# Kernel optimization log

Hardware: AMD Instinct MI355X
Metric: run time of the kernel (lower is better)

The kernel has to match this reference:

```python
import jax, jax.numpy as jnp
import numpy as np

N = 50000   # nodes
E = 600000  # edges (avg degree 12)
F = 16      # raw node features
P = 32      # n_channels_preproc
C = 128     # n_channels
L = 6       # n_gnn_layers
LBL = 2     # n_labels


def _dense_init(k, fan_in, shape):
    return (jax.random.normal(k, shape, jnp.float32) / np.float32(np.sqrt(fan_in)))


def setup_inputs() -> dict:
    key = jax.random.key(0)
    ks = jax.random.split(key, 12)
    return {
        "x": jax.random.normal(ks[0], (N, F), jnp.float32),
        "edge_src": jax.random.randint(ks[1], (E,), 0, N, dtype=jnp.int32),
        "edge_dst": jax.random.randint(ks[2], (E,), 0, N, dtype=jnp.int32),
        "edge_weight": jax.random.uniform(ks[3], (E,), jnp.float32),  # normalized-adjacency values
        "preproc_W": _dense_init(ks[4], F, (F, P)), "preproc_b": jnp.zeros((P,), jnp.float32),
        "fc_in1_W": _dense_init(ks[5], P, (P, C)), "fc_in1_b": jnp.zeros((C,), jnp.float32),
        "fc_in2_W": _dense_init(ks[6], P, (P, C)), "fc_in2_b": jnp.zeros((C,), jnp.float32),
        "gcn_W": _dense_init(ks[7], C, (L, C, C)), "gcn_b": jnp.zeros((L, C), jnp.float32),
        "fcg_W": _dense_init(ks[8], 2 * C, (L, 2 * C, C)), "fcg_b": jnp.zeros((L, C), jnp.float32),
        "last1_W": _dense_init(ks[9], 2 * C, (2 * C, C)), "last1_b": jnp.zeros((C,), jnp.float32),
        "last2_W": _dense_init(ks[10], C, (C, LBL)), "last2_b": jnp.zeros((LBL,), jnp.float32),
    }


def reference(x, edge_src, edge_dst, edge_weight,
              preproc_W, preproc_b, fc_in1_W, fc_in1_b, fc_in2_W, fc_in2_b,
              gcn_W, gcn_b, fcg_W, fcg_b, last1_W, last1_b, last2_W, last2_b):
    relu = jax.nn.relu
    h = relu(x @ preproc_W + preproc_b)                      # preproc Dense
    node_id = relu(h @ fc_in1_W + fc_in1_b)                  # node identity branch
    h = relu(h @ fc_in2_W + fc_in2_b)

    def layer(h, params):
        W, b, Wf, bf = params
        # GCNConv: act(A_hat @ (h @ W) + b), A_hat as COO edge list
        hw = h @ W                                           # [N, C]
        msg = hw[edge_src] * edge_weight[:, None]            # [E, C]
        agg = jax.ops.segment_sum(msg, edge_dst, num_segments=N)
        g = relu(agg + b)
        merged = jnp.concatenate([node_id, g], axis=-1)      # [N, 2C]
        return relu(merged @ Wf + bf), None                  # dropout = identity (eval)

    h, _ = jax.lax.scan(layer, h, (gcn_W, gcn_b, fcg_W, fcg_b))

    merged = jnp.concatenate([node_id, h], axis=-1)
    h = relu(merged @ last1_W + last1_b)
    return jax.nn.sigmoid(h @ last2_W + last2_b)             # [N, n_labels]
```

## Files before the change

kernel.cpp:

```cpp
#include <hip/hip_runtime.h>
#include <cstddef>
#include <cstdint>

#define NN 50000
#define NE 600000
#define SCAN_BLOCKS ((NN + 1023) / 1024)

typedef __attribute__((ext_vector_type(8))) short bf16x8;
typedef __attribute__((ext_vector_type(4))) float f32x4;

#define SWZ(x) (((x) ^ ((x) >> 2)) & 3)

__device__ __forceinline__ float bf2f(ushort u) {
    return __uint_as_float(((uint32_t)u) << 16);
}
__device__ __forceinline__ ushort f2bf(float f) {
    uint32_t b = __float_as_uint(f);
    return (ushort)((b + 0x7FFF + ((b >> 16) & 1)) >> 16);
}

__global__ __launch_bounds__(256)
void convert_weights(const float* __restrict__ f1W, const float* __restrict__ f2W,
                     const float* __restrict__ gW, const float* __restrict__ fgW,
                     const float* __restrict__ l1W, ushort* __restrict__ wt)
{
    int i = blockIdx.x * 256 + threadIdx.x;
    if (i >= 335872) return;
    float v;
    if (i < 4096) {
        int c = i >> 5, k = i & 31;
        v = f1W[k * 128 + c];
    } else if (i < 8192) {
        int j = i - 4096; int c = j >> 5, k = j & 31;
        v = f2W[k * 128 + c];
    } else if (i < 8192 + 98304) {
        int j = i - 8192; int l = j >> 14, r = j & 16383;
        int c = r >> 7, k = r & 127;
        v = gW[l * 16384 + k * 128 + c];
    } else if (i < 8192 + 98304 + 196608) {
        int j = i - (8192 + 98304); int l = j >> 15, r = j & 32767;
        int c = r >> 8, k = r & 255;
        v = fgW[l * 32768 + k * 128 + c];
    } else {
        int j = i - (8192 + 98304 + 196608);
        int c = j >> 8, k = j & 255;
        v = l1W[k * 128 + c];
    }
    wt[i] = f2bf(v);
}

__global__ __launch_bounds__(256)
void preproc_kernel(const float* __restrict__ x, const float* __restrict__ W,
                    const float* __restrict__ b, ushort* __restrict__ out)
{
    __shared__ float Wl[512];
    __shared__ float bl[32];
    int tx = threadIdx.x;
    Wl[tx]       = W[tx];
    Wl[tx + 256] = W[tx + 256];
    if (tx < 32) bl[tx] = b[tx];
    __syncthreads();
    int n = blockIdx.x * 256 + tx;
    if (n >= NN) return;
    float xr[16];
    const float4* xp = (const float4*)(x + (size_t)n * 16);
#pragma unroll
    for (int q = 0; q < 4; ++q) {
        float4 v = xp[q];
        xr[q*4+0]=v.x; xr[q*4+1]=v.y; xr[q*4+2]=v.z; xr[q*4+3]=v.w;
    }
    float acc[32];
#pragma unroll
    for (int c = 0; c < 32; ++c) acc[c] = bl[c];
#pragma unroll
    for (int k = 0; k < 16; ++k)
#pragma unroll
        for (int c = 0; c < 32; ++c)
            acc[c] = fmaf(xr[k], Wl[k*32+c], acc[c]);
    ushort4* op = (ushort4*)(out + (size_t)n * 32);
#pragma unroll
    for (int q = 0; q < 8; ++q) {
        ushort4 v;
        v.x = f2bf(fmaxf(acc[q*4+0], 0.f));
        v.y = f2bf(fmaxf(acc[q*4+1], 0.f));
        v.z = f2bf(fmaxf(acc[q*4+2], 0.f));
        v.w = f2bf(fmaxf(acc[q*4+3], 0.f));
        op[q] = v;
    }
}

__global__ __launch_bounds__(128)
void gemm_mfma(const ushort* __restrict__ A1, int K1,
               const ushort* __restrict__ Wt, const float* __restrict__ bias,
               ushort* __restrict__ out, int nrows)
{
    __shared__ ushort Atile[64 * 32];
    __shared__ ushort Btile[128 * 32];
    const int tx   = threadIdx.x;
    const int wave = tx >> 6;
    const int lane = tx & 63;
    const int bm   = blockIdx.x * 64;
    const int Ktot = K1;

    const int rs  = lane >> 2;
    const int chn = (lane & 3) ^ SWZ(rs);
    const int m    = lane & 15;
    const int quad = lane >> 4;
    const int slot = quad ^ SWZ(m);

    f32x4 acc0[8], acc1[8];
#pragma unroll
    for (int t = 0; t < 8; ++t) {
        acc0[t] = (f32x4){0.f, 0.f, 0.f, 0.f};
        acc1[t] = (f32x4){0.f, 0.f, 0.f, 0.f};
    }

    for (int kk = 0; kk < Ktot; kk += 32) {
#pragma unroll
        for (int i = 0; i < 2; ++i) {
            int seg = wave + 2 * i;
            int row = seg * 16 + rs;
            int ar  = bm + row; if (ar >= nrows) ar = nrows - 1;
            __builtin_amdgcn_global_load_lds(
                (const __attribute__((address_space(1))) void*)
                    (A1 + (size_t)ar * K1 + kk + chn * 8),
                (__attribute__((address_space(3))) void*)(Atile + seg * 512),
                16, 0, 0);
        }
#pragma unroll
        for (int i = 0; i < 4; ++i) {
            int seg = wave + 2 * i;
            int col = seg * 16 + rs;
            __builtin_amdgcn_global_load_lds(
                (const __attribute__((address_space(1))) void*)
                    (Wt + (size_t)col * Ktot + kk + chn * 8),
                (__attribute__((address_space(3))) void*)(Btile + seg * 512),
                16, 0, 0);
        }
        __syncthreads();
        bf16x8 af0 = *(const bf16x8*)(Atile + (wave * 32 + m) * 32 + slot * 8);
        bf16x8 af1 = *(const bf16x8*)(Atile + (wave * 32 + 16 + m) * 32 + slot * 8);
#pragma unroll
        for (int t = 0; t < 8; ++t) {
            bf16x8 bfr = *(const bf16x8*)(Btile + (t * 16 + m) * 32 + slot * 8);
            acc0[t] = __builtin_amdgcn_mfma_f32_16x16x32_bf16(af0, bfr, acc0[t], 0, 0, 0);
            acc1[t] = __builtin_amdgcn_mfma_f32_16x16x32_bf16(af1, bfr, acc1[t], 0, 0, 0);
        }
        __syncthreads();
    }

#pragma unroll
    for (int half = 0; half < 2; ++half) {
        const int orow0 = bm + wave * 32 + half * 16 + quad * 4;
#pragma unroll
        for (int t = 0; t < 8; ++t) {
            int col = t * 16 + m;
            float bb = bias[col];
            f32x4 a = half ? acc1[t] : acc0[t];
#pragma unroll
            for (int r = 0; r < 4; ++r) {
                int row = orow0 + r;
                if (row < nrows)
                    out[(size_t)row * 128 + col] = f2bf(fmaxf(a[r] + bb, 0.f));
            }
        }
    }
}

__global__ __launch_bounds__(128)
void gemm_fused(const ushort* __restrict__ A1, int K1,
                const ushort* __restrict__ A2, int K2,
                const ushort* __restrict__ Wt, const float* __restrict__ bias,
                const ushort* __restrict__ Wg,
                ushort* __restrict__ out_hw, int nrows)
{
    __shared__ ushort Atile[64 * 32];
    __shared__ ushort Btile[128 * 32];
    __shared__ ushort Xt[64 * 128];
    const int tx   = threadIdx.x;
    const int wave = tx >> 6;
    const int lane = tx & 63;
    const int bm   = blockIdx.x * 64;
    const int Ktot = K1 + K2;

    const int rs  = lane >> 2;
    const int chn = (lane & 3) ^ SWZ(rs);
    const int m    = lane & 15;
    const int quad = lane >> 4;
    const int slot = quad ^ SWZ(m);

    f32x4 acc0[8], acc1[8];
#pragma unroll
    for (int t = 0; t < 8; ++t) {
        acc0[t] = (f32x4){0.f, 0.f, 0.f, 0.f};
        acc1[t] = (f32x4){0.f, 0.f, 0.f, 0.f};
    }

    for (int kk = 0; kk < Ktot; kk += 32) {
        const ushort* asrc; int astr, kl;
        if (kk < K1) { asrc = A1; astr = K1; kl = kk; }
        else         { asrc = A2; astr = K2; kl = kk - K1; }
#pragma unroll
        for (int i = 0; i < 2; ++i) {
            int seg = wave + 2 * i;
            int row = seg * 16 + rs;
            int ar  = bm + row; if (ar >= nrows) ar = nrows - 1;
            __builtin_amdgcn_global_load_lds(
                (const __attribute__((address_space(1))) void*)
                    (asrc + (size_t)ar * astr + kl + chn * 8),
                (__attribute__((address_space(3))) void*)(Atile + seg * 512),
                16, 0, 0);
        }
#pragma unroll
        for (int i = 0; i < 4; ++i) {
            int seg = wave + 2 * i;
            int col = seg * 16 + rs;
            __builtin_amdgcn_global_load_lds(
                (const __attribute__((address_space(1))) void*)
                    (Wt + (size_t)col * Ktot + kk + chn * 8),
                (__attribute__((address_space(3))) void*)(Btile + seg * 512),
                16, 0, 0);
        }
        __syncthreads();
        bf16x8 af0 = *(const bf16x8*)(Atile + (wave * 32 + m) * 32 + slot * 8);
        bf16x8 af1 = *(const bf16x8*)(Atile + (wave * 32 + 16 + m) * 32 + slot * 8);
#pragma unroll
        for (int t = 0; t < 8; ++t) {
            bf16x8 bfr = *(const bf16x8*)(Btile + (t * 16 + m) * 32 + slot * 8);
            acc0[t] = __builtin_amdgcn_mfma_f32_16x16x32_bf16(af0, bfr, acc0[t], 0, 0, 0);
            acc1[t] = __builtin_amdgcn_mfma_f32_16x16x32_bf16(af1, bfr, acc1[t], 0, 0, 0);
        }
        __syncthreads();
    }

#pragma unroll
    for (int half = 0; half < 2; ++half) {
        int rbase = wave * 32 + half * 16 + quad * 4;
#pragma unroll
        for (int t = 0; t < 8; ++t) {
            int col = t * 16 + m;
            float bb = bias[col];
            int c32 = col >> 5, within = col & 7, ks = (col >> 3) & 3;
            f32x4 a = half ? acc1[t] : acc0[t];
#pragma unroll
            for (int r = 0; r < 4; ++r) {
                int row = rbase + r;
                int pos = ks ^ SWZ(row & 15);
                Xt[row * 128 + c32 * 32 + pos * 8 + within] =
                    f2bf(fmaxf(a[r] + bb, 0.f));
            }
        }
    }
#pragma unroll
    for (int t = 0; t < 8; ++t) {
        acc0[t] = (f32x4){0.f, 0.f, 0.f, 0.f};
        acc1[t] = (f32x4){0.f, 0.f, 0.f, 0.f};
    }
    __syncthreads();

    for (int c32 = 0; c32 < 4; ++c32) {
        int kk = c32 * 32;
#pragma unroll
        for (int i = 0; i < 4; ++i) {
            int seg = wave + 2 * i;
            int col = seg * 16 + rs;
            __builtin_amdgcn_global_load_lds(
                (const __attribute__((address_space(1))) void*)
                    (Wg + (size_t)col * 128 + kk + chn * 8),
                (__attribute__((address_space(3))) void*)(Btile + seg * 512),
                16, 0, 0);
        }
        __syncthreads();
        bf16x8 af0 = *(const bf16x8*)(Xt + (wave * 32 + m) * 128 + kk + slot * 8);
        bf16x8 af1 = *(const bf16x8*)(Xt + (wave * 32 + 16 + m) * 128 + kk + slot * 8);
#pragma unroll
        for (int t = 0; t < 8; ++t) {
            bf16x8 bfr = *(const bf16x8*)(Btile + (t * 16 + m) * 32 + slot * 8);
            acc0[t] = __builtin_amdgcn_mfma_f32_16x16x32_bf16(af0, bfr, acc0[t], 0, 0, 0);
            acc1[t] = __builtin_amdgcn_mfma_f32_16x16x32_bf16(af1, bfr, acc1[t], 0, 0, 0);
        }
        __syncthreads();
    }

#pragma unroll
    for (int half = 0; half < 2; ++half) {
        const int orow0 = bm + wave * 32 + half * 16 + quad * 4;
#pragma unroll
        for (int t = 0; t < 8; ++t) {
            int col = t * 16 + m;
            f32x4 a = half ? acc1[t] : acc0[t];
#pragma unroll
            for (int r = 0; r < 4; ++r) {
                int row = orow0 + r;
                if (row < nrows)
                    out_hw[(size_t)row * 128 + col] = f2bf(a[r]);
            }
        }
    }
}

__global__ __launch_bounds__(128)
void gemm_last(const ushort* __restrict__ nid, const ushort* __restrict__ agg,
               const ushort* __restrict__ Wt, const float* __restrict__ bias5,
               const ushort* __restrict__ Wl1, const float* __restrict__ l1b,
               const float* __restrict__ l2W, const float* __restrict__ l2b,
               float* __restrict__ out, int nrows)
{
    __shared__ ushort Atile[64 * 32];
    __shared__ ushort Btile[128 * 32];
    __shared__ ushort Xt[64 * 128];
    __shared__ float  w2s[256];
    const int tx   = threadIdx.x;
    const int wave = tx >> 6;
    const int lane = tx & 63;
    const int bm   = blockIdx.x * 64;

    w2s[tx]       = l2W[tx];
    w2s[tx + 128] = l2W[tx + 128];

    const int rs  = lane >> 2;
    const int chn = (lane & 3) ^ SWZ(rs);
    const int m    = lane & 15;
    const int quad = lane >> 4;
    const int slot = quad ^ SWZ(m);

    f32x4 acc0[8], acc1[8];
#pragma unroll
    for (int t = 0; t < 8; ++t) {
        acc0[t] = (f32x4){0.f, 0.f, 0.f, 0.f};
        acc1[t] = (f32x4){0.f, 0.f, 0.f, 0.f};
    }

    for (int kk = 0; kk < 256; kk += 32) {
        const ushort* asrc; int kl;
        if (kk < 128) { asrc = nid; kl = kk; }
        else          { asrc = agg; kl = kk - 128; }
#pragma unroll
        for (int i = 0; i < 2; ++i) {
            int seg = wave + 2 * i;
            int row = seg * 16 + rs;
            int ar  = bm + row; if (ar >= nrows) ar = nrows - 1;
            __builtin_amdgcn_global_load_lds(
                (const __attribute__((address_space(1))) void*)
                    (asrc + (size_t)ar * 128 + kl + chn * 8),
                (__attribute__((address_space(3))) void*)(Atile + seg * 512),
                16, 0, 0);
        }
#pragma unroll
        for (int i = 0; i < 4; ++i) {
            int seg = wave + 2 * i;
            int col = seg * 16 + rs;
            __builtin_amdgcn_global_load_lds(
                (const __attribute__((address_space(1))) void*)
                    (Wt + (size_t)col * 256 + kk + chn * 8),
                (__attribute__((address_space(3))) void*)(Btile + seg * 512),
                16, 0, 0);
        }
        __syncthreads();
        bf16x8 af0 = *(const bf16x8*)(Atile + (wave * 32 + m) * 32 + slot * 8);
        bf16x8 af1 = *(const bf16x8*)(Atile + (wave * 32 + 16 + m) * 32 + slot * 8);
#pragma unroll
        for (int t = 0; t < 8; ++t) {
            bf16x8 bfr = *(const bf16x8*)(Btile + (t * 16 + m) * 32 + slot * 8);
            acc0[t] = __builtin_amdgcn_mfma_f32_16x16x32_bf16(af0, bfr, acc0[t], 0, 0, 0);
            acc1[t] = __builtin_amdgcn_mfma_f32_16x16x32_bf16(af1, bfr, acc1[t], 0, 0, 0);
        }
        __syncthreads();
    }

#pragma unroll
    for (int half = 0; half < 2; ++half) {
        int rbase = wave * 32 + half * 16 + quad * 4;
#pragma unroll
        for (int t = 0; t < 8; ++t) {
            int col = t * 16 + m;
            float bb = bias5[col];
            int c32 = col >> 5, within = col & 7, ks = (col >> 3) & 3;
            f32x4 a = half ? acc1[t] : acc0[t];
#pragma unroll
            for (int r = 0; r < 4; ++r) {
                int row = rbase + r;
                int pos = ks ^ SWZ(row & 15);
                Xt[row * 128 + c32 * 32 + pos * 8 + within] =
                    f2bf(fmaxf(a[r] + bb, 0.f));
            }
        }
    }
#pragma unroll
    for (int t = 0; t < 8; ++t) {
        acc0[t] = (f32x4){0.f, 0.f, 0.f, 0.f};
        acc1[t] = (f32x4){0.f, 0.f, 0.f, 0.f};
    }
    __syncthreads();

    for (int c8 = 0; c8 < 8; ++c8) {
        int kk = c8 * 32;
        if (c8 < 4) {
#pragma unroll
            for (int i = 0; i < 2; ++i) {
                int seg = wave + 2 * i;
                int row = seg * 16 + rs;
                int ar  = bm + row; if (ar >= nrows) ar = nrows - 1;
                __builtin_amdgcn_global_load_lds(
                    (const __attribute__((address_space(1))) void*)
                        (nid + (size_t)ar * 128 + kk + chn * 8),
                    (__attribute__((address_space(3))) void*)(Atile + seg * 512),
                    16, 0, 0);
            }
        }
#pragma unroll
        for (int i = 0; i < 4; ++i) {
            int seg = wave + 2 * i;
            int col = seg * 16 + rs;
            __builtin_amdgcn_global_load_lds(
                (const __attribute__((address_space(1))) void*)
                    (Wl1 + (size_t)col * 256 + kk + chn * 8),
                (__attribute__((address_space(3))) void*)(Btile + seg * 512),
                16, 0, 0);
        }
        __syncthreads();
        bf16x8 af0, af1;
        if (c8 < 4) {
            af0 = *(const bf16x8*)(Atile + (wave * 32 + m) * 32 + slot * 8);
            af1 = *(const bf16x8*)(Atile + (wave * 32 + 16 + m) * 32 + slot * 8);
        } else {
            int ko = (c8 - 4) * 32;
            af0 = *(const bf16x8*)(Xt + (wave * 32 + m) * 128 + ko + slot * 8);
            af1 = *(const bf16x8*)(Xt + (wave * 32 + 16 + m) * 128 + ko + slot * 8);
        }
#pragma unroll
        for (int t = 0; t < 8; ++t) {
            bf16x8 bfr = *(const bf16x8*)(Btile + (t * 16 + m) * 32 + slot * 8);
            acc0[t] = __builtin_amdgcn_mfma_f32_16x16x32_bf16(af0, bfr, acc0[t], 0, 0, 0);
            acc1[t] = __builtin_amdgcn_mfma_f32_16x16x32_bf16(af1, bfr, acc1[t], 0, 0, 0);
        }
        __syncthreads();
    }

    float bb[8];
#pragma unroll
    for (int t = 0; t < 8; ++t) bb[t] = l1b[t * 16 + m];
    float b20 = l2b[0], b21 = l2b[1];
#pragma unroll
    for (int half = 0; half < 2; ++half) {
#pragma unroll
        for (int r = 0; r < 4; ++r) {
            float p0 = 0.f, p1 = 0.f;
#pragma unroll
            for (int t = 0; t < 8; ++t) {
                int col = t * 16 + m;
                f32x4 a = half ? acc1[t] : acc0[t];
                float v = fmaxf(a[r] + bb[t], 0.f);
                p0 = fmaf(v, w2s[col * 2 + 0], p0);
                p1 = fmaf(v, w2s[col * 2 + 1], p1);
            }
#pragma unroll
            for (int mask = 1; mask < 16; mask <<= 1) {
                p0 += __shfl_xor(p0, mask);
                p1 += __shfl_xor(p1, mask);
            }
            if (m == 0) {
                int row = bm + wave * 32 + half * 16 + quad * 4 + r;
                if (row < nrows) {
                    out[(size_t)row * 2 + 0] = 1.f / (1.f + __expf(-(p0 + b20)));
                    out[(size_t)row * 2 + 1] = 1.f / (1.f + __expf(-(p1 + b21)));
                }
            }
        }
    }
}

__global__ __launch_bounds__(256)
void hist_kernel(const int* __restrict__ dst, int* __restrict__ deg)
{
    int e = blockIdx.x * 256 + threadIdx.x;
    if (e < NE) atomicAdd(&deg[dst[e]], 1);
}

__global__ __launch_bounds__(1024)
void scan1_kernel(const int* __restrict__ deg, int* __restrict__ off,
                  int* __restrict__ bsum)
{
    __shared__ int buf[1024];
    int tx = threadIdx.x;
    int i = blockIdx.x * 1024 + tx;
    int v = (i < NN) ? deg[i] : 0;
    buf[tx] = v;
    __syncthreads();
    for (int s = 1; s < 1024; s <<= 1) {
        int t = (tx >= s) ? buf[tx - s] : 0;
        __syncthreads();
        buf[tx] += t;
        __syncthreads();
    }
    if (i < NN) off[i] = buf[tx] - v;
    if (tx == 1023) bsum[blockIdx.x] = buf[1023];
}

__global__ __launch_bounds__(64)
void scan2_kernel(int* __restrict__ bsum)
{
    __shared__ int buf[64];
    int tx = threadIdx.x;
    int v = (tx < SCAN_BLOCKS) ? bsum[tx] : 0;
    buf[tx] = v;
    __syncthreads();
    for (int s = 1; s < 64; s <<= 1) {
        int t = (tx >= s) ? buf[tx - s] : 0;
        __syncthreads();
        buf[tx] += t;
        __syncthreads();
    }
    if (tx < SCAN_BLOCKS) bsum[tx] = buf[tx] - v;
}

__global__ __launch_bounds__(1024)
void scan3_kernel(int* __restrict__ off, const int* __restrict__ bsum)
{
    int i = blockIdx.x * 1024 + threadIdx.x;
    if (i < NN) off[i] += bsum[blockIdx.x];
    if (i == 0) off[NN] = NE;
}

__global__ __launch_bounds__(256)
void permute_kernel(const int* __restrict__ src, const int* __restrict__ dst,
                    const float* __restrict__ w, const int* __restrict__ off,
                    int* __restrict__ cursor, unsigned long long* __restrict__ esw)
{
    int e = blockIdx.x * 256 + threadIdx.x;
    if (e >= NE) return;
    int d = dst[e];
    int p = off[d] + atomicAdd(&cursor[d], 1);
    unsigned long long packed = (unsigned int)src[e] |
        ((unsigned long long)(unsigned int)__float_as_uint(w[e]) << 32);
    __builtin_nontemporal_store(packed, &esw[p]);
}

__global__ __launch_bounds__(256)
void gather_agg(const ushort* __restrict__ hw,
                const unsigned long long* __restrict__ esw,
                const int* __restrict__ off, const float* __restrict__ gbias,
                ushort* __restrict__ agg)
{
    const int wid  = blockIdx.x * 4 + (threadIdx.x >> 6);
    const int lane = threadIdx.x & 63;
    if (wid >= NN) return;
    const int e0 = off[wid], e1 = off[wid + 1];
    float a0 = 0.f, a1 = 0.f, b0 = 0.f, b1 = 0.f;
    const ushort* hp = hw + lane * 2;
    for (int base = e0; base < e1; base += 64) {
        int idx = base + lane;
        unsigned long long pk = (idx < e1) ? esw[idx] : 0ULL;
        int slo = (int)(unsigned int)(pk & 0xffffffffULL);
        int shi = (int)(unsigned int)(pk >> 32);
        int cnt = e1 - base; if (cnt > 64) cnt = 64;
        int cnt8 = (cnt + 7) & ~7;
        for (int j = 0; j < cnt8; j += 8) {
            int   ss[8];
            float ww[8];
            unsigned int rv[8];
#pragma unroll
            for (int k = 0; k < 8; ++k) {
                ss[k] = __builtin_amdgcn_readlane(slo, j + k);
                ww[k] = __int_as_float(__builtin_amdgcn_readlane(shi, j + k));
            }
#pragma unroll
            for (int k = 0; k < 8; ++k)
                rv[k] = *(const unsigned int*)(hp + (size_t)ss[k] * 128);
#pragma unroll
            for (int k = 0; k < 8; k += 2) {
                a0 = fmaf(bf2f((ushort)(rv[k]   & 0xffff)), ww[k],   a0);
                a1 = fmaf(bf2f((ushort)(rv[k]   >> 16)),    ww[k],   a1);
                b0 = fmaf(bf2f((ushort)(rv[k+1] & 0xffff)), ww[k+1], b0);
                b1 = fmaf(bf2f((ushort)(rv[k+1] >> 16)),    ww[k+1], b1);
            }
        }
    }
    a0 += b0; a1 += b1;
    float g0 = gbias[lane * 2], g1 = gbias[lane * 2 + 1];
    unsigned int o = (unsigned int)f2bf(fmaxf(a0 + g0, 0.f)) |
                     ((unsigned int)f2bf(fmaxf(a1 + g1, 0.f)) << 16);
    *(unsigned int*)(agg + (size_t)wid * 128 + lane * 2) = o;
}

extern "C" void kernel_launch(void* const* d_in, const int* in_sizes, int n_in,
                              void* d_out, int out_size, void* d_ws, size_t ws_size,
                              hipStream_t stream)
{
    const float* x    = (const float*)d_in[0];
    const int*   esrc = (const int*)  d_in[1];
    const int*   edst = (const int*)  d_in[2];
    const float* ew   = (const float*)d_in[3];
    const float* preW = (const float*)d_in[4];
    const float* preb = (const float*)d_in[5];
    const float* f1W  = (const float*)d_in[6];
    const float* f1b  = (const float*)d_in[7];
    const float* f2W  = (const float*)d_in[8];
    const float* f2b  = (const float*)d_in[9];
    const float* gW   = (const float*)d_in[10];
    const float* gb   = (const float*)d_in[11];
    const float* fgW  = (const float*)d_in[12];
    const float* fgb  = (const float*)d_in[13];
    const float* l1W  = (const float*)d_in[14];
    const float* l1b  = (const float*)d_in[15];
    const float* l2W  = (const float*)d_in[16];
    const float* l2b  = (const float*)d_in[17];
    float* out = (float*)d_out;

    ushort* wt   = (ushort*)d_ws;
    ushort* wf1  = wt;
    ushort* wf2  = wf1 + 4096;
    ushort* wg   = wf2 + 4096;
    ushort* wfg  = wg  + 98304;
    ushort* wl1  = wfg + 196608;
    ushort* h0b  = wl1 + 32768;
    ushort* nidb = h0b  + (size_t)NN * 32;
    ushort* hwb  = nidb + (size_t)NN * 128;
    ushort* aggb = hwb  + (size_t)NN * 128;
    ushort* endu = aggb + (size_t)NN * 128;
    unsigned long long* esw = (unsigned long long*)(((uintptr_t)endu + 15) & ~(uintptr_t)15);
    int*   deg   = (int*)(esw + NE);
    int*   off   = deg + NN;
    int*   cursor= off + NN + 1;
    int*   bsum  = cursor + NN;

    const int gblocks = (NN + 63) / 64;
    const int eblocks = (NE + 255) / 256;
    const int wblocks = (NN + 3) / 4;

    convert_weights<<<(335872 + 255) / 256, 256, 0, stream>>>(f1W, f2W, gW, fgW, l1W, wt);

    hipMemsetAsync(deg, 0, (size_t)NN * sizeof(int), stream);
    hipMemsetAsync(cursor, 0, (size_t)NN * sizeof(int), stream);
    hist_kernel<<<eblocks, 256, 0, stream>>>(edst, deg);
    scan1_kernel<<<SCAN_BLOCKS, 1024, 0, stream>>>(deg, off, bsum);
    scan2_kernel<<<1, 64, 0, stream>>>(bsum);
    scan3_kernel<<<SCAN_BLOCKS, 1024, 0, stream>>>(off, bsum);
    permute_kernel<<<eblocks, 256, 0, stream>>>(esrc, edst, ew, off, cursor, esw);

    preproc_kernel<<<(NN + 255) / 256, 256, 0, stream>>>(x, preW, preb, h0b);
    gemm_mfma<<<gblocks, 128, 0, stream>>>(h0b, 32, wf1, f1b, nidb, NN);
    gemm_fused<<<gblocks, 128, 0, stream>>>(h0b, 32, nullptr, 0, wf2, f2b,
                                            wg, hwb, NN);
    for (int l = 0; l < 6; ++l) {
        gather_agg<<<wblocks, 256, 0, stream>>>(hwb, esw, off,
                                                gb + (size_t)l * 128, aggb);
        if (l < 5) {
            gemm_fused<<<gblocks, 128, 0, stream>>>(nidb, 128, aggb, 128,
                                                    wfg + (size_t)l * 32768,
                                                    fgb + (size_t)l * 128,
                                                    wg + (size_t)(l + 1) * 16384,
                                                    hwb, NN);
        }
    }
    gemm_last<<<gblocks, 128, 0, stream>>>(nidb, aggb,
                                           wfg + (size_t)5 * 32768,
                                           fgb + (size_t)5 * 128,
                                           wl1, l1b, l2W, l2b, out, NN);
}
```

Before: 462.3 us.

## Enlarge fused GEMM tile to 128 rows and pack edges into 32-bit words

The fused GEMM now handles 128 rows per block, with each wave computing four 16-row MFMA fragments. This reuses each B tile load across twice as many rows, at the cost of more accumulator registers, more LDS and half as many blocks. Separately, the CSR edge records shrink from 64-bit (src index plus fp32 weight) to 32-bit (17-bit src plus bf16 weight), halving edge-stream traffic in the gather. The edge weight is now rounded to bf16, and the encoding relies on node indices fitting in 17 bits.

```diff
diff --git a/kernel.cpp b/kernel.cpp
--- a/kernel.cpp
+++ b/kernel.cpp
@@ -174,13 +174,13 @@
                 const ushort* __restrict__ Wg,
                 ushort* __restrict__ out_hw, int nrows)
 {
-    __shared__ ushort Atile[64 * 32];
+    __shared__ ushort Atile[128 * 32];
     __shared__ ushort Btile[128 * 32];
-    __shared__ ushort Xt[64 * 128];
+    __shared__ ushort Xt[128 * 128];
     const int tx   = threadIdx.x;
     const int wave = tx >> 6;
     const int lane = tx & 63;
-    const int bm   = blockIdx.x * 64;
+    const int bm   = blockIdx.x * 128;
     const int Ktot = K1 + K2;
 
     const int rs  = lane >> 2;
@@ -189,19 +189,18 @@
     const int quad = lane >> 4;
     const int slot = quad ^ SWZ(m);
 
-    f32x4 acc0[8], acc1[8];
-#pragma unroll
-    for (int t = 0; t < 8; ++t) {
-        acc0[t] = (f32x4){0.f, 0.f, 0.f, 0.f};
-        acc1[t] = (f32x4){0.f, 0.f, 0.f, 0.f};
-    }
+    f32x4 acc[4][8];
+#pragma unroll
+    for (int r = 0; r < 4; ++r)
+#pragma unroll
+        for (int t = 0; t < 8; ++t) acc[r][t] = (f32x4){0.f, 0.f, 0.f, 0.f};
 
     for (int kk = 0; kk < Ktot; kk += 32) {
         const ushort* asrc; int astr, kl;
         if (kk < K1) { asrc = A1; astr = K1; kl = kk; }
         else         { asrc = A2; astr = K2; kl = kk - K1; }
 #pragma unroll
-        for (int i = 0; i < 2; ++i) {
+        for (int i = 0; i < 4; ++i) {
             int seg = wave + 2 * i;
             int row = seg * 16 + rs;
             int ar  = bm + row; if (ar >= nrows) ar = nrows - 1;
@@ -222,40 +221,41 @@
                 16, 0, 0);
         }
         __syncthreads();
-        bf16x8 af0 = *(const bf16x8*)(Atile + (wave * 32 + m) * 32 + slot * 8);
-        bf16x8 af1 = *(const bf16x8*)(Atile + (wave * 32 + 16 + m) * 32 + slot * 8);
+        bf16x8 af[4];
+#pragma unroll
+        for (int r = 0; r < 4; ++r)
+            af[r] = *(const bf16x8*)(Atile + (wave * 64 + r * 16 + m) * 32 + slot * 8);
 #pragma unroll
         for (int t = 0; t < 8; ++t) {
             bf16x8 bfr = *(const bf16x8*)(Btile + (t * 16 + m) * 32 + slot * 8);
-            acc0[t] = __builtin_amdgcn_mfma_f32_16x16x32_bf16(af0, bfr, acc0[t], 0, 0, 0);
-            acc1[t] = __builtin_amdgcn_mfma_f32_16x16x32_bf16(af1, bfr, acc1[t], 0, 0, 0);
-        }
-        __syncthreads();
-    }
-
-#pragma unroll
-    for (int half = 0; half < 2; ++half) {
-        int rbase = wave * 32 + half * 16 + quad * 4;
+#pragma unroll
+            for (int r = 0; r < 4; ++r)
+                acc[r][t] = __builtin_amdgcn_mfma_f32_16x16x32_bf16(af[r], bfr, acc[r][t], 0, 0, 0);
+        }
+        __syncthreads();
+    }
+
+#pragma unroll
+    for (int r = 0; r < 4; ++r) {
+        int rbase = wave * 64 + r * 16 + quad * 4;
 #pragma unroll
         for (int t = 0; t < 8; ++t) {
             int col = t * 16 + m;
             float bb = bias[col];
             int c32 = col >> 5, within = col & 7, ks = (col >> 3) & 3;
-            f32x4 a = half ? acc1[t] : acc0[t];
-#pragma unroll
-            for (int r = 0; r < 4; ++r) {
-                int row = rbase + r;
+#pragma unroll
+            for (int q = 0; q < 4; ++q) {
+                int row = rbase + q;
                 int pos = ks ^ SWZ(row & 15);
                 Xt[row * 128 + c32 * 32 + pos * 8 + within] =
-                    f2bf(fmaxf(a[r] + bb, 0.f));
-            }
-        }
-    }
-#pragma unroll
-    for (int t = 0; t < 8; ++t) {
-        acc0[t] = (f32x4){0.f, 0.f, 0.f, 0.f};
-        acc1[t] = (f32x4){0.f, 0.f, 0.f, 0.f};
-    }
+                    f2bf(fmaxf(acc[r][t][q] + bb, 0.f));
+            }
+        }
+    }
+#pragma unroll
+    for (int r = 0; r < 4; ++r)
+#pragma unroll
+        for (int t = 0; t < 8; ++t) acc[r][t] = (f32x4){0.f, 0.f, 0.f, 0.f};
     __syncthreads();
 
     for (int c32 = 0; c32 < 4; ++c32) {
@@ -271,29 +271,31 @@
                 16, 0, 0);
         }
         __syncthreads();
-        bf16x8 af0 = *(const bf16x8*)(Xt + (wave * 32 + m) * 128 + kk + slot * 8);
-        bf16x8 af1 = *(const bf16x8*)(Xt + (wave * 32 + 16 + m) * 128 + kk + slot * 8);
+        bf16x8 af[4];
+#pragma unroll
+        for (int r = 0; r < 4; ++r)
+            af[r] = *(const bf16x8*)(Xt + (wave * 64 + r * 16 + m) * 128 + kk + slot * 8);
 #pragma unroll
         for (int t = 0; t < 8; ++t) {
             bf16x8 bfr = *(const bf16x8*)(Btile + (t * 16 + m) * 32 + slot * 8);
-            acc0[t] = __builtin_amdgcn_mfma_f32_16x16x32_bf16(af0, bfr, acc0[t], 0, 0, 0);
-            acc1[t] = __builtin_amdgcn_mfma_f32_16x16x32_bf16(af1, bfr, acc1[t], 0, 0, 0);
-        }
-        __syncthreads();
-    }
-
-#pragma unroll
-    for (int half = 0; half < 2; ++half) {
-        const int orow0 = bm + wave * 32 + half * 16 + quad * 4;
+#pragma unroll
+            for (int r = 0; r < 4; ++r)
+                acc[r][t] = __builtin_amdgcn_mfma_f32_16x16x32_bf16(af[r], bfr, acc[r][t], 0, 0, 0);
+        }
+        __syncthreads();
+    }
+
+#pragma unroll
+    for (int r = 0; r < 4; ++r) {
+        const int orow0 = bm + wave * 64 + r * 16 + quad * 4;
 #pragma unroll
         for (int t = 0; t < 8; ++t) {
             int col = t * 16 + m;
-            f32x4 a = half ? acc1[t] : acc0[t];
-#pragma unroll
-            for (int r = 0; r < 4; ++r) {
-                int row = orow0 + r;
+#pragma unroll
+            for (int q = 0; q < 4; ++q) {
+                int row = orow0 + q;
                 if (row < nrows)
-                    out_hw[(size_t)row * 128 + col] = f2bf(a[r]);
+                    out_hw[(size_t)row * 128 + col] = f2bf(acc[r][t][q]);
             }
         }
     }
@@ -525,20 +527,20 @@
 __global__ __launch_bounds__(256)
 void permute_kernel(const int* __restrict__ src, const int* __restrict__ dst,
                     const float* __restrict__ w, const int* __restrict__ off,
-                    int* __restrict__ cursor, unsigned long long* __restrict__ esw)
+                    int* __restrict__ cursor, unsigned int* __restrict__ esw)
 {
     int e = blockIdx.x * 256 + threadIdx.x;
     if (e >= NE) return;
     int d = dst[e];
     int p = off[d] + atomicAdd(&cursor[d], 1);
-    unsigned long long packed = (unsigned int)src[e] |
-        ((unsigned long long)(unsigned int)__float_as_uint(w[e]) << 32);
+    unsigned int packed = (unsigned int)src[e] |
+                          ((unsigned int)f2bf(w[e]) << 17);
     __builtin_nontemporal_store(packed, &esw[p]);
 }
 
 __global__ __launch_bounds__(256)
 void gather_agg(const ushort* __restrict__ hw,
-                const unsigned long long* __restrict__ esw,
+                const unsigned int* __restrict__ esw,
                 const int* __restrict__ off, const float* __restrict__ gbias,
                 ushort* __restrict__ agg)
 {
@@ -550,29 +552,26 @@
     const ushort* hp = hw + lane * 2;
     for (int base = e0; base < e1; base += 64) {
         int idx = base + lane;
-        unsigned long long pk = (idx < e1) ? esw[idx] : 0ULL;
-        int slo = (int)(unsigned int)(pk & 0xffffffffULL);
-        int shi = (int)(unsigned int)(pk >> 32);
+        int pk = (idx < e1) ? (int)esw[idx] : 0;
         int cnt = e1 - base; if (cnt > 64) cnt = 64;
         int cnt8 = (cnt + 7) & ~7;
         for (int j = 0; j < cnt8; j += 8) {
-            int   ss[8];
-            float ww[8];
+            int pp[8];
             unsigned int rv[8];
 #pragma unroll
-            for (int k = 0; k < 8; ++k) {
-                ss[k] = __builtin_amdgcn_readlane(slo, j + k);
-                ww[k] = __int_as_float(__builtin_amdgcn_readlane(shi, j + k));
-            }
-#pragma unroll
             for (int k = 0; k < 8; ++k)
-                rv[k] = *(const unsigned int*)(hp + (size_t)ss[k] * 128);
+                pp[k] = __builtin_amdgcn_readlane(pk, j + k);
+#pragma unroll
+            for (int k = 0; k < 8; ++k)
+                rv[k] = *(const unsigned int*)(hp + (size_t)(pp[k] & 0x1FFFF) * 128);
 #pragma unroll
             for (int k = 0; k < 8; k += 2) {
-                a0 = fmaf(bf2f((ushort)(rv[k]   & 0xffff)), ww[k],   a0);
-                a1 = fmaf(bf2f((ushort)(rv[k]   >> 16)),    ww[k],   a1);
-                b0 = fmaf(bf2f((ushort)(rv[k+1] & 0xffff)), ww[k+1], b0);
-                b1 = fmaf(bf2f((ushort)(rv[k+1] >> 16)),    ww[k+1], b1);
+                float w0 = bf2f((ushort)((unsigned int)pp[k]   >> 17));
+                float w1 = bf2f((ushort)((unsigned int)pp[k+1] >> 17));
+                a0 = fmaf(bf2f((ushort)(rv[k]   & 0xffff)), w0, a0);
+                a1 = fmaf(bf2f((ushort)(rv[k]   >> 16)),    w0, a1);
+                b0 = fmaf(bf2f((ushort)(rv[k+1] & 0xffff)), w1, b0);
+                b1 = fmaf(bf2f((ushort)(rv[k+1] >> 16)),    w1, b1);
             }
         }
     }
@@ -618,15 +617,16 @@
     ushort* hwb  = nidb + (size_t)NN * 128;
     ushort* aggb = hwb  + (size_t)NN * 128;
     ushort* endu = aggb + (size_t)NN * 128;
-    unsigned long long* esw = (unsigned long long*)(((uintptr_t)endu + 15) & ~(uintptr_t)15);
+    unsigned int* esw = (unsigned int*)(((uintptr_t)endu + 15) & ~(uintptr_t)15);
     int*   deg   = (int*)(esw + NE);
     int*   off   = deg + NN;
     int*   cursor= off + NN + 1;
     int*   bsum  = cursor + NN;
 
-    const int gblocks = (NN + 63) / 64;
-    const int eblocks = (NE + 255) / 256;
-    const int wblocks = (NN + 3) / 4;
+    const int gblocks  = (NN + 63) / 64;
+    const int gblocks2 = (NN + 127) / 128;
+    const int eblocks  = (NE + 255) / 256;
+    const int wblocks  = (NN + 3) / 4;
 
     convert_weights<<<(335872 + 255) / 256, 256, 0, stream>>>(f1W, f2W, gW, fgW, l1W, wt);
 
@@ -640,17 +640,17 @@
 
     preproc_kernel<<<(NN + 255) / 256, 256, 0, stream>>>(x, preW, preb, h0b);
     gemm_mfma<<<gblocks, 128, 0, stream>>>(h0b, 32, wf1, f1b, nidb, NN);
-    gemm_fused<<<gblocks, 128, 0, stream>>>(h0b, 32, nullptr, 0, wf2, f2b,
-                                            wg, hwb, NN);
+    gemm_fused<<<gblocks2, 128, 0, stream>>>(h0b, 32, nullptr, 0, wf2, f2b,
+                                             wg, hwb, NN);
     for (int l = 0; l < 6; ++l) {
         gather_agg<<<wblocks, 256, 0, stream>>>(hwb, esw, off,
                                                 gb + (size_t)l * 128, aggb);
         if (l < 5) {
-            gemm_fused<<<gblocks, 128, 0, stream>>>(nidb, 128, aggb, 128,
-                                                    wfg + (size_t)l * 32768,
-                                                    fgb + (size_t)l * 128,
-                                                    wg + (size_t)(l + 1) * 16384,
-                                                    hwb, NN);
+            gemm_fused<<<gblocks2, 128, 0, stream>>>(nidb, 128, aggb, 128,
+                                                     wfg + (size_t)l * 32768,
+                                                     fgb + (size_t)l * 128,
+                                                     wg + (size_t)(l + 1) * 16384,
+                                                     hwb, NN);
         }
     }
     gemm_last<<<gblocks, 128, 0, stream>>>(nidb, aggb,
```

New measurement: 480.1 us. 3.9% more time.

## Pack edges into 32 bits and process eight nodes per wave in gather

Applied to the files above, without the earlier changes.

Edge records shrink from 64-bit (src, fp32 weight) to 32-bit, holding a 17-bit source index and a bf16 weight in the high bits. Each wavefront now walks the contiguous CSR range of eight destination nodes, so edge-index chunk loads are fully used across node boundaries rather than partly idle for low-degree nodes. Rounding the edge weight to bf16 reduces precision, and the per-edge boundary check adds branching inside the inner loop.

```diff
diff --git a/kernel.cpp b/kernel.cpp
--- a/kernel.cpp
+++ b/kernel.cpp
@@ -525,62 +525,73 @@
 __global__ __launch_bounds__(256)
 void permute_kernel(const int* __restrict__ src, const int* __restrict__ dst,
                     const float* __restrict__ w, const int* __restrict__ off,
-                    int* __restrict__ cursor, unsigned long long* __restrict__ esw)
+                    int* __restrict__ cursor, unsigned int* __restrict__ esw)
 {
     int e = blockIdx.x * 256 + threadIdx.x;
     if (e >= NE) return;
     int d = dst[e];
     int p = off[d] + atomicAdd(&cursor[d], 1);
-    unsigned long long packed = (unsigned int)src[e] |
-        ((unsigned long long)(unsigned int)__float_as_uint(w[e]) << 32);
+    unsigned int packed = (unsigned int)src[e] |
+                          ((unsigned int)f2bf(w[e]) << 17);
     __builtin_nontemporal_store(packed, &esw[p]);
 }
 
 __global__ __launch_bounds__(256)
 void gather_agg(const ushort* __restrict__ hw,
-                const unsigned long long* __restrict__ esw,
+                const unsigned int* __restrict__ esw,
                 const int* __restrict__ off, const float* __restrict__ gbias,
                 ushort* __restrict__ agg)
 {
-    const int wid  = blockIdx.x * 4 + (threadIdx.x >> 6);
+    const int g    = blockIdx.x * 4 + (threadIdx.x >> 6);
     const int lane = threadIdx.x & 63;
-    if (wid >= NN) return;
-    const int e0 = off[wid], e1 = off[wid + 1];
-    float a0 = 0.f, a1 = 0.f, b0 = 0.f, b1 = 0.f;
+    int n = g * 8;
+    if (n >= NN) return;
+    int n_end = n + 8; if (n_end > NN) n_end = NN;
+    const int base = off[n];
+    const int end  = off[n_end];
+    int nb = off[n + 1];
     const ushort* hp = hw + lane * 2;
-    for (int base = e0; base < e1; base += 64) {
-        int idx = base + lane;
-        unsigned long long pk = (idx < e1) ? esw[idx] : 0ULL;
-        int slo = (int)(unsigned int)(pk & 0xffffffffULL);
-        int shi = (int)(unsigned int)(pk >> 32);
-        int cnt = e1 - base; if (cnt > 64) cnt = 64;
+    const float g0 = gbias[lane * 2], g1 = gbias[lane * 2 + 1];
+    float a0 = 0.f, a1 = 0.f;
+
+    for (int chunk = base; chunk < end; chunk += 64) {
+        int idx = chunk + lane;
+        int pk = (idx < end) ? (int)esw[idx] : 0;
+        int cnt = end - chunk; if (cnt > 64) cnt = 64;
         int cnt8 = (cnt + 7) & ~7;
         for (int j = 0; j < cnt8; j += 8) {
-            int   ss[8];
-            float ww[8];
+            int pp[8];
             unsigned int rv[8];
 #pragma unroll
+            for (int k = 0; k < 8; ++k)
+                pp[k] = __builtin_amdgcn_readlane(pk, j + k);
+#pragma unroll
+            for (int k = 0; k < 8; ++k)
+                rv[k] = *(const unsigned int*)(hp + (size_t)(pp[k] & 0x1FFFF) * 128);
+#pragma unroll
             for (int k = 0; k < 8; ++k) {
-                ss[k] = __builtin_amdgcn_readlane(slo, j + k);
-                ww[k] = __int_as_float(__builtin_amdgcn_readlane(shi, j + k));
-            }
-#pragma unroll
-            for (int k = 0; k < 8; ++k)
-                rv[k] = *(const unsigned int*)(hp + (size_t)ss[k] * 128);
-#pragma unroll
-            for (int k = 0; k < 8; k += 2) {
-                a0 = fmaf(bf2f((ushort)(rv[k]   & 0xffff)), ww[k],   a0);
-                a1 = fmaf(bf2f((ushort)(rv[k]   >> 16)),    ww[k],   a1);
-                b0 = fmaf(bf2f((ushort)(rv[k+1] & 0xffff)), ww[k+1], b0);
-                b1 = fmaf(bf2f((ushort)(rv[k+1] >> 16)),    ww[k+1], b1);
-            }
-        }
-    }
-    a0 += b0; a1 += b1;
-    float g0 = gbias[lane * 2], g1 = gbias[lane * 2 + 1];
-    unsigned int o = (unsigned int)f2bf(fmaxf(a0 + g0, 0.f)) |
-                     ((unsigned int)f2bf(fmaxf(a1 + g1, 0.f)) << 16);
-    *(unsigned int*)(agg + (size_t)wid * 128 + lane * 2) = o;
+                int e = chunk + j + k;
+                while (e == nb) {
+                    unsigned int o = (unsigned int)f2bf(fmaxf(a0 + g0, 0.f)) |
+                                     ((unsigned int)f2bf(fmaxf(a1 + g1, 0.f)) << 16);
+                    *(unsigned int*)(agg + (size_t)n * 128 + lane * 2) = o;
+                    a0 = 0.f; a1 = 0.f;
+                    ++n;
+                    nb = (n < n_end) ? off[n + 1] : 0x7fffffff;
+                }
+                float w = bf2f((ushort)((unsigned int)pp[k] >> 17));
+                a0 = fmaf(bf2f((ushort)(rv[k] & 0xffff)), w, a0);
+                a1 = fmaf(bf2f((ushort)(rv[k] >> 16)),    w, a1);
+            }
+        }
+    }
+    while (n < n_end) {
+        unsigned int o = (unsigned int)f2bf(fmaxf(a0 + g0, 0.f)) |
+                         ((unsigned int)f2bf(fmaxf(a1 + g1, 0.f)) << 16);
+        *(unsigned int*)(agg + (size_t)n * 128 + lane * 2) = o;
+        a0 = 0.f; a1 = 0.f;
+        ++n;
+    }
 }
 
 extern "C" void kernel_launch(void* const* d_in, const int* in_sizes, int n_in,
@@ -618,7 +629,7 @@
     ushort* hwb  = nidb + (size_t)NN * 128;
     ushort* aggb = hwb  + (size_t)NN * 128;
     ushort* endu = aggb + (size_t)NN * 128;
-    unsigned long long* esw = (unsigned long long*)(((uintptr_t)endu + 15) & ~(uintptr_t)15);
+    unsigned int* esw = (unsigned int*)(((uintptr_t)endu + 15) & ~(uintptr_t)15);
     int*   deg   = (int*)(esw + NE);
     int*   off   = deg + NN;
     int*   cursor= off + NN + 1;
@@ -626,7 +637,8 @@
 
     const int gblocks = (NN + 63) / 64;
     const int eblocks = (NE + 255) / 256;
-    const int wblocks = (NN + 3) / 4;
+    const int ngroups = (NN + 7) / 8;
+    const int wblocks = (ngroups + 3) / 4;
 
     convert_weights<<<(335872 + 255) / 256, 256, 0, stream>>>(f1W, f2W, gW, fgW, l1W, wt);
 
```

After: 451.8 us. -2.3%, faster.
